# Performance work log

Measured on AMD Instinct MI355X. Metric: run time of the kernel, lower is better.

## Reference

```python
import jax, jax.numpy as jnp
import numpy as np

B, C, D, W, H = 2, 256, 16, 32, 32
CS = 256          # in_channels_style
SN = 256          # number of style tokens
HEADS = 8
DH = C // HEADS
EPS = 1e-6


def setup_inputs() -> dict:
    key = jax.random.key(0)
    ks = jax.random.split(key, 8)
    x = jax.random.normal(ks[0], (B, C, D, W, H), dtype=jnp.float32)
    s = jax.random.normal(ks[1], (B, SN, CS), dtype=jnp.float32)
    # learned parameters
    ln_w = jnp.ones((C,), jnp.float32)
    ln_b = jnp.zeros((C,), jnp.float32)
    lns_w = jnp.ones((CS,), jnp.float32)
    lns_b = jnp.zeros((CS,), jnp.float32)
    sc = 0.02
    Wq = jax.random.normal(ks[2], (C, C), jnp.float32) * sc   # (out, in) 1x1 conv3d
    Wk = jax.random.normal(ks[3], (C, CS), jnp.float32) * sc  # Linear weight (out, in)
    Wv = jax.random.normal(ks[4], (C, CS), jnp.float32) * sc
    Wo = jax.random.normal(ks[5], (C, C), jnp.float32) * sc   # proj_out 1x1 conv3d
    bo = jnp.zeros((C,), jnp.float32)
    return {"x": x, "s": s, "ln_w": ln_w, "ln_b": ln_b, "lns_w": lns_w,
            "lns_b": lns_b, "Wq": Wq, "Wk": Wk, "Wv": Wv, "Wo": Wo, "bo": bo}


def reference(x, s, ln_w, ln_b, lns_w, lns_b, Wq, Wk, Wv, Wo, bo):
    b = x.shape[0]
    # channels_first LayerNorm over channel dim (dim 1) of 5D tensor
    u = x.mean(axis=1, keepdims=True)
    var = ((x - u) ** 2).mean(axis=1, keepdims=True)
    hn = (x - u) / jnp.sqrt(var + EPS)
    hn = ln_w[None, :, None, None, None] * hn + ln_b[None, :, None, None, None]
    # standard LayerNorm on last dim of style tokens
    mu = s.mean(axis=-1, keepdims=True)
    sv = ((s - mu) ** 2).mean(axis=-1, keepdims=True)
    sn = (s - mu) / jnp.sqrt(sv + EPS) * lns_w + lns_b
    # projections: 1x1 conv3d == channel matmul; linears on style
    q = jnp.einsum('bcdwh,oc->bodwh', hn, Wq)               # (B,C,D,W,H)
    k = jnp.einsum('bnc,oc->bon', sn, Wk)                    # (B,C,Sn)
    v = jnp.einsum('bnc,oc->bon', sn, Wv)                    # (B,C,Sn)
    d, w, h = q.shape[2], q.shape[3], q.shape[4]
    N = d * w * h
    q = q.reshape(b * HEADS, DH, N).transpose(0, 2, 1)       # (B*h, N, dh)
    k = k.reshape(b * HEADS, DH, SN)                         # (B*h, dh, Sn)
    v = v.reshape(b * HEADS, DH, SN)                         # (B*h, dh, Sn)
    scores = jnp.einsum('bnd,bds->bns', q, k) * (DH ** -0.5)
    attn = jax.nn.softmax(scores, axis=2)                    # (B*h, N, Sn)
    out = jnp.einsum('bds,bns->bdn', v, attn)                # (B*h, dh, N)
    out = out.reshape(b, C, d, w, h)
    out = jnp.einsum('bcdwh,oc->bodwh', out, Wo) + bo[None, :, None, None, None]
    return x + out
```

## Files before the change

kernel.cpp:

```cpp
#include <hip/hip_runtime.h>

#define EPS_ 1e-6f

typedef __attribute__((ext_vector_type(8))) short bf16x8;
typedef __attribute__((ext_vector_type(4))) float f32x4;

__device__ __forceinline__ unsigned short f2b(float f){
  union { float f; unsigned int u; } v; v.f = f;
  unsigned int r = v.u + 0x7fffu + ((v.u >> 16) & 1u);
  return (unsigned short)(r >> 16);
}
__device__ __forceinline__ unsigned int packrne(float a, float b){
  return (unsigned int)f2b(a) | ((unsigned int)f2b(b) << 16);
}
__device__ __forceinline__ unsigned int packtr(float a, float b){
  return (__float_as_uint(a) >> 16) | (__float_as_uint(b) & 0xffff0000u);
}
union cvt8 { unsigned int u[4]; bf16x8 v; };

__global__ __launch_bounds__(256) void k_prep(
    const float* __restrict__ Wq, const float* __restrict__ Wk,
    const float* __restrict__ Wv, const float* __restrict__ Wo,
    const float* __restrict__ s, const float* __restrict__ lns_w,
    const float* __restrict__ lns_b,
    unsigned short* __restrict__ bWq, unsigned short* __restrict__ bWo,
    unsigned short* __restrict__ Kb, unsigned short* __restrict__ Vb){
  __shared__ unsigned short snb[64*264];
  int t = threadIdx.x;
  int blk = blockIdx.x;
  if (blk < 256){
    int i = blk*256 + t;
    bWq[i] = f2b(Wq[i]);
    bWo[i] = f2b(Wo[i]);
    return;
  }
  int idx = blk - 256;
  int b = idx >> 3, n0 = ((idx >> 1) & 3) * 64, mat = idx & 1;
  int tok = t >> 2, sub = t & 3;
  {
    const float4* srow = (const float4*)(s + ((size_t)(b*256 + n0 + tok))*256 + sub*64);
    float4 vv[16];
    float s1 = 0.f, s2 = 0.f;
    #pragma unroll
    for (int j=0;j<16;++j){
      float4 v = srow[j]; vv[j] = v;
      s1 += (v.x+v.y)+(v.z+v.w);
      s2 += (v.x*v.x+v.y*v.y)+(v.z*v.z+v.w*v.w);
    }
    s1 += __shfl_xor(s1,1); s1 += __shfl_xor(s1,2);
    s2 += __shfl_xor(s2,1); s2 += __shfl_xor(s2,2);
    float mu = s1*(1.f/256.f);
    float rstd = rsqrtf(s2*(1.f/256.f) - mu*mu + EPS_);
    const float4* wr = (const float4*)(lns_w + sub*64);
    const float4* br = (const float4*)(lns_b + sub*64);
    #pragma unroll
    for (int j=0;j<16;++j){
      float4 v = vv[j], g = wr[j], o = br[j];
      float n0v = (v.x-mu)*rstd*g.x + o.x;
      float n1v = (v.y-mu)*rstd*g.y + o.y;
      float n2v = (v.z-mu)*rstd*g.z + o.z;
      float n3v = (v.w-mu)*rstd*g.w + o.w;
      uint2 pk = { packrne(n0v,n1v), packrne(n2v,n3v) };
      *(uint2*)&snb[tok*264 + sub*64 + j*4] = pk;
    }
  }
  __syncthreads();
  int lane = t & 63, w = t >> 6, quad = lane >> 4, l16 = lane & 15;
  const float* W = mat ? Wv : Wk;
  f32x4 acc[4][4];
  #pragma unroll
  for (int ot=0;ot<4;++ot)
    #pragma unroll
    for (int nt=0;nt<4;++nt) acc[ot][nt] = (f32x4){0.f,0.f,0.f,0.f};
  for (int ks=0; ks<8; ++ks){
    bf16x8 afr[4], bfr[4];
    #pragma unroll
    for (int ot=0;ot<4;++ot){
      const float4* wr = (const float4*)(W + (size_t)(w*64 + ot*16 + l16)*256 + ks*32 + quad*8);
      float4 a0 = wr[0], a1 = wr[1];
      cvt8 cv;
      cv.u[0]=packrne(a0.x,a0.y); cv.u[1]=packrne(a0.z,a0.w);
      cv.u[2]=packrne(a1.x,a1.y); cv.u[3]=packrne(a1.z,a1.w);
      afr[ot] = cv.v;
    }
    #pragma unroll
    for (int nt=0;nt<4;++nt)
      bfr[nt] = *(const bf16x8*)&snb[(nt*16+l16)*264 + ks*32 + quad*8];
    #pragma unroll
    for (int ot=0;ot<4;++ot)
      #pragma unroll
      for (int nt=0;nt<4;++nt)
        acc[ot][nt] = __builtin_amdgcn_mfma_f32_16x16x32_bf16(afr[ot], bfr[nt], acc[ot][nt], 0,0,0);
  }
  #pragma unroll
  for (int ot=0;ot<4;++ot){
    int otg = w*4 + ot;
    int h = otg >> 1, dbase = (otg&1)*16 + quad*4;
    #pragma unroll
    for (int nt=0;nt<4;++nt){
      int n = n0 + nt*16 + l16;
      if (!mat){
        uint2 pk = { packrne(acc[ot][nt][0], acc[ot][nt][1]),
                     packrne(acc[ot][nt][2], acc[ot][nt][3]) };
        *(uint2*)&Kb[(((size_t)(b*8+h))*256 + n)*32 + dbase] = pk;
      } else {
        #pragma unroll
        for (int r=0;r<4;++r)
          Vb[(((size_t)(b*8+h))*32 + dbase + r)*256 + n] = f2b(acc[ot][nt][r]);
      }
    }
  }
}

__global__ __launch_bounds__(256,4) void k_mega(
    const float* __restrict__ x, const float* __restrict__ ln_w,
    const float* __restrict__ ln_b,
    const unsigned short* __restrict__ bWq, const unsigned short* __restrict__ bWo,
    const unsigned short* __restrict__ Kb, const unsigned short* __restrict__ Vb,
    const float* __restrict__ bo, float* __restrict__ out){
  __shared__ unsigned short buf1[32*264];
  __shared__ float st[512];
  int t = threadIdx.x;
  int blk = blockIdx.x;
  int b = blk >> 9, p0 = (blk & 511) << 5;
  int pp = t & 31, seg = t >> 5;
  const float* xb = x + ((size_t)b << 22) + p0 + pp;

  float s1=0.f, s2=0.f;
  for (int k=0;k<16;++k){
    int c = seg*32 + 2*k;
    float v0 = xb[(size_t)c << 14], v1 = xb[(size_t)(c+1) << 14];
    s1 += v0+v1; s2 += v0*v0+v1*v1;
    *(unsigned int*)&buf1[pp*264 + c] = packrne(v0, v1);
  }
  st[seg*32+pp] = s1; st[256+seg*32+pp] = s2;
  __syncthreads();
  float a=0.f, q=0.f;
  #pragma unroll
  for (int g=0; g<8; ++g){ a += st[g*32+pp]; q += st[256+g*32+pp]; }
  float mu = a*(1.f/256.f);
  float rstd = rsqrtf(q*(1.f/256.f) - mu*mu + EPS_);
  for (int k=0;k<16;++k){
    int c = seg*32 + 2*k;
    unsigned int pk = *(unsigned int*)&buf1[pp*264 + c];
    float v0 = __uint_as_float(pk << 16);
    float v1 = __uint_as_float(pk & 0xffff0000u);
    v0 = (v0-mu)*rstd*ln_w[c]   + ln_b[c];
    v1 = (v1-mu)*rstd*ln_w[c+1] + ln_b[c+1];
    *(unsigned int*)&buf1[pp*264 + c] = packrne(v0, v1);
  }
  __syncthreads();

  int lane = t & 63, w = t >> 6, quad = lane >> 4, l16 = lane & 15;
  int ptile = w & 1, ohalf = w >> 1;
  int prow = ptile*16 + l16;
  const float qs = 0.17677669529663689f * 1.44269504088896341f;

  {
    f32x4 acc[4][2];
    #pragma unroll
    for (int ot=0;ot<4;++ot)
      #pragma unroll
      for (int pt=0;pt<2;++pt) acc[ot][pt] = (f32x4){0.f,0.f,0.f,0.f};
    const unsigned short* wq = bWq + (size_t)(w*64 + l16)*256 + quad*8;
    #pragma unroll 2
    for (int ks=0; ks<8; ++ks){
      bf16x8 bfr[2], afr[4];
      #pragma unroll
      for (int ot=0;ot<4;++ot)
        afr[ot] = *(const bf16x8*)(wq + (size_t)ot*16*256 + ks*32);
      #pragma unroll
      for (int pt=0;pt<2;++pt)
        bfr[pt] = *(const bf16x8*)&buf1[(pt*16+l16)*264 + ks*32 + quad*8];
      #pragma unroll
      for (int ot=0;ot<4;++ot)
        #pragma unroll
        for (int pt=0;pt<2;++pt)
          acc[ot][pt] = __builtin_amdgcn_mfma_f32_16x16x32_bf16(afr[ot], bfr[pt], acc[ot][pt], 0,0,0);
    }
    __syncthreads();
    #pragma unroll
    for (int ot=0;ot<4;++ot){
      int o = w*64 + ot*16 + quad*4;
      #pragma unroll
      for (int pt=0;pt<2;++pt){
        uint2 pk = { packrne(acc[ot][pt][0]*qs, acc[ot][pt][1]*qs),
                     packrne(acc[ot][pt][2]*qs, acc[ot][pt][3]*qs) };
        *(uint2*)&buf1[(pt*16+l16)*264 + o] = pk;
      }
    }
  }
  __syncthreads();

  int srcA = ((( 2*quad   )&3)<<4) + l16;
  int srcB = (((2*quad + 1)&3)<<4) + l16;
  bool hiq = quad >= 2;
  bf16x8 qf[4];
  #pragma unroll
  for (int hh=0;hh<4;++hh)
    qf[hh] = *(const bf16x8*)&buf1[prow*264 + (ohalf*4+hh)*32 + quad*8];

  for (int hh=0; hh<4; ++hh){
    int h = ohalf*4 + hh;
    int bh = b*8 + h;
    const unsigned short* kb = Kb + (size_t)bh*8192 + quad*8;
    const unsigned short* vb = Vb + (size_t)bh*8192 + quad*8;
    f32x4 av[2] = {{0.f,0.f,0.f,0.f},{0.f,0.f,0.f,0.f}};
    float sm0=0.f, sm1=0.f, sm2=0.f, sm3=0.f;
    #pragma unroll 2
    for (int ks=0; ks<8; ++ks){
      bf16x8 kf0 = *(const bf16x8*)(kb + (size_t)((2*ks  )*16+l16)*32);
      bf16x8 kf1 = *(const bf16x8*)(kb + (size_t)((2*ks+1)*16+l16)*32);
      bf16x8 vf0 = *(const bf16x8*)(vb + (size_t)(     l16)*256 + ks*32);
      bf16x8 vf1 = *(const bf16x8*)(vb + (size_t)(16 + l16)*256 + ks*32);
      f32x4 z = {0.f,0.f,0.f,0.f};
      f32x4 s0 = __builtin_amdgcn_mfma_f32_16x16x32_bf16(kf0, qf[hh], z, 0,0,0);
      f32x4 s1 = __builtin_amdgcn_mfma_f32_16x16x32_bf16(kf1, qf[hh], z, 0,0,0);
      float e00 = exp2f(s0[0]), e01 = exp2f(s0[1]);
      float e02 = exp2f(s0[2]), e03 = exp2f(s0[3]);
      float e10 = exp2f(s1[0]), e11 = exp2f(s1[1]);
      float e12 = exp2f(s1[2]), e13 = exp2f(s1[3]);
      sm0 += e00 + e10; sm1 += e01 + e11;
      sm2 += e02 + e12; sm3 += e03 + e13;
      unsigned int p00 = packtr(e00, e01), p01 = packtr(e02, e03);
      unsigned int p10 = packtr(e10, e11), p11 = packtr(e12, e13);
      unsigned int aA0 = (unsigned int)__shfl((int)p00, srcA);
      unsigned int aB0 = (unsigned int)__shfl((int)p10, srcA);
      unsigned int aA1 = (unsigned int)__shfl((int)p01, srcA);
      unsigned int aB1 = (unsigned int)__shfl((int)p11, srcA);
      unsigned int bA0 = (unsigned int)__shfl((int)p00, srcB);
      unsigned int bB0 = (unsigned int)__shfl((int)p10, srcB);
      unsigned int bA1 = (unsigned int)__shfl((int)p01, srcB);
      unsigned int bB1 = (unsigned int)__shfl((int)p11, srcB);
      cvt8 cv;
      cv.u[0] = hiq ? aB0 : aA0;
      cv.u[1] = hiq ? aB1 : aA1;
      cv.u[2] = hiq ? bB0 : bA0;
      cv.u[3] = hiq ? bB1 : bA1;
      bf16x8 pf = cv.v;
      av[0] = __builtin_amdgcn_mfma_f32_16x16x32_bf16(vf0, pf, av[0], 0,0,0);
      av[1] = __builtin_amdgcn_mfma_f32_16x16x32_bf16(vf1, pf, av[1], 0,0,0);
    }
    float sm = (sm0+sm1)+(sm2+sm3);
    sm += __shfl_xor(sm, 16);
    sm += __shfl_xor(sm, 32);
    float inv = 1.f/sm;
    #pragma unroll
    for (int dt=0; dt<2; ++dt){
      uint2 pko = { packrne(av[dt][0]*inv, av[dt][1]*inv),
                    packrne(av[dt][2]*inv, av[dt][3]*inv) };
      *(uint2*)&buf1[prow*264 + h*32 + dt*16 + quad*4] = pko;
    }
  }
  __syncthreads();

  {
    f32x4 oacc[4][2];
    #pragma unroll
    for (int ot=0;ot<4;++ot)
      #pragma unroll
      for (int pt=0;pt<2;++pt) oacc[ot][pt] = (f32x4){0.f,0.f,0.f,0.f};
    const unsigned short* wo = bWo + (size_t)(w*64 + l16)*256 + quad*8;
    #pragma unroll 2
    for (int ks=0; ks<8; ++ks){
      bf16x8 bfr[2], afr[4];
      #pragma unroll
      for (int ot=0;ot<4;++ot)
        afr[ot] = *(const bf16x8*)(wo + (size_t)ot*16*256 + ks*32);
      #pragma unroll
      for (int pt=0;pt<2;++pt)
        bfr[pt] = *(const bf16x8*)&buf1[(pt*16+l16)*264 + ks*32 + quad*8];
      #pragma unroll
      for (int ot=0;ot<4;++ot)
        #pragma unroll
        for (int pt=0;pt<2;++pt)
          oacc[ot][pt] = __builtin_amdgcn_mfma_f32_16x16x32_bf16(afr[ot], bfr[pt], oacc[ot][pt], 0,0,0);
    }
    #pragma unroll
    for (int ot=0;ot<4;++ot){
      int o = w*64 + ot*16 + quad*4;
      #pragma unroll
      for (int pt=0;pt<2;++pt){
        int p = p0 + pt*16 + l16;
        #pragma unroll
        for (int r=0;r<4;++r){
          size_t idx = (((size_t)b*256 + o + r) << 14) + p;
          out[idx] = oacc[ot][pt][r] + bo[o+r] + x[idx];
        }
      }
    }
  }
}

extern "C" void kernel_launch(void* const* d_in, const int* in_sizes, int n_in,
                              void* d_out, int out_size, void* d_ws, size_t ws_size,
                              hipStream_t stream) {
  const float* x     = (const float*)d_in[0];
  const float* s     = (const float*)d_in[1];
  const float* ln_w  = (const float*)d_in[2];
  const float* ln_b  = (const float*)d_in[3];
  const float* lns_w = (const float*)d_in[4];
  const float* lns_b = (const float*)d_in[5];
  const float* Wq    = (const float*)d_in[6];
  const float* Wk    = (const float*)d_in[7];
  const float* Wv    = (const float*)d_in[8];
  const float* Wo    = (const float*)d_in[9];
  const float* bo    = (const float*)d_in[10];
  float* out = (float*)d_out;

  unsigned short* bWq = (unsigned short*)d_ws;
  unsigned short* bWo = bWq + 65536;
  unsigned short* Kb  = bWo + 65536;
  unsigned short* Vb  = Kb + 131072;

  k_prep<<<272,  256, 0, stream>>>(Wq, Wk, Wv, Wo, s, lns_w, lns_b, bWq, bWo, Kb, Vb);
  k_mega<<<1024, 256, 0, stream>>>(x, ln_w, ln_b, bWq, bWo, Kb, Vb, bo, out);
}
```

Measured before the change: 191.1 us.

## Halve pixel tile per block to raise occupancy and drop a barrier

Shrinks each block's pixel tile from 32 to 16 positions, doubles the grid, and raises launch bounds to 8 blocks per CU. Each wave now handles two heads across all 16 rows instead of four heads on half the rows, so one block barrier after the Q projection can be dropped. The aim is more resident waves to hide memory and MFMA latency. In exchange, the Wq/Wo weight fragments are loaded twice as often per pixel, and the MFMA work per loaded fragment is reduced.

```diff
diff --git a/kernel.cpp b/kernel.cpp
--- a/kernel.cpp
+++ b/kernel.cpp
@@ -112,36 +112,36 @@
   }
 }
 
-__global__ __launch_bounds__(256,4) void k_mega(
+__global__ __launch_bounds__(256,8) void k_mega(
     const float* __restrict__ x, const float* __restrict__ ln_w,
     const float* __restrict__ ln_b,
     const unsigned short* __restrict__ bWq, const unsigned short* __restrict__ bWo,
     const unsigned short* __restrict__ Kb, const unsigned short* __restrict__ Vb,
     const float* __restrict__ bo, float* __restrict__ out){
-  __shared__ unsigned short buf1[32*264];
+  __shared__ unsigned short buf1[16*264];
   __shared__ float st[512];
   int t = threadIdx.x;
   int blk = blockIdx.x;
-  int b = blk >> 9, p0 = (blk & 511) << 5;
-  int pp = t & 31, seg = t >> 5;
+  int b = blk >> 10, p0 = (blk & 1023) << 4;
+  int pp = t & 15, seg = t >> 4;
   const float* xb = x + ((size_t)b << 22) + p0 + pp;
 
   float s1=0.f, s2=0.f;
-  for (int k=0;k<16;++k){
-    int c = seg*32 + 2*k;
+  for (int k=0;k<8;++k){
+    int c = seg*16 + 2*k;
     float v0 = xb[(size_t)c << 14], v1 = xb[(size_t)(c+1) << 14];
     s1 += v0+v1; s2 += v0*v0+v1*v1;
     *(unsigned int*)&buf1[pp*264 + c] = packrne(v0, v1);
   }
-  st[seg*32+pp] = s1; st[256+seg*32+pp] = s2;
+  st[seg*16+pp] = s1; st[256+seg*16+pp] = s2;
   __syncthreads();
   float a=0.f, q=0.f;
   #pragma unroll
-  for (int g=0; g<8; ++g){ a += st[g*32+pp]; q += st[256+g*32+pp]; }
+  for (int g=0; g<16; ++g){ a += st[g*16+pp]; q += st[256+g*16+pp]; }
   float mu = a*(1.f/256.f);
   float rstd = rsqrtf(q*(1.f/256.f) - mu*mu + EPS_);
-  for (int k=0;k<16;++k){
-    int c = seg*32 + 2*k;
+  for (int k=0;k<8;++k){
+    int c = seg*16 + 2*k;
     unsigned int pk = *(unsigned int*)&buf1[pp*264 + c];
     float v0 = __uint_as_float(pk << 16);
     float v1 = __uint_as_float(pk & 0xffff0000u);
@@ -152,56 +152,44 @@
   __syncthreads();
 
   int lane = t & 63, w = t >> 6, quad = lane >> 4, l16 = lane & 15;
-  int ptile = w & 1, ohalf = w >> 1;
-  int prow = ptile*16 + l16;
   const float qs = 0.17677669529663689f * 1.44269504088896341f;
 
   {
-    f32x4 acc[4][2];
-    #pragma unroll
-    for (int ot=0;ot<4;++ot)
-      #pragma unroll
-      for (int pt=0;pt<2;++pt) acc[ot][pt] = (f32x4){0.f,0.f,0.f,0.f};
+    f32x4 acc[4];
+    #pragma unroll
+    for (int ot=0;ot<4;++ot) acc[ot] = (f32x4){0.f,0.f,0.f,0.f};
     const unsigned short* wq = bWq + (size_t)(w*64 + l16)*256 + quad*8;
     #pragma unroll 2
     for (int ks=0; ks<8; ++ks){
-      bf16x8 bfr[2], afr[4];
+      bf16x8 afr[4];
       #pragma unroll
       for (int ot=0;ot<4;++ot)
         afr[ot] = *(const bf16x8*)(wq + (size_t)ot*16*256 + ks*32);
-      #pragma unroll
-      for (int pt=0;pt<2;++pt)
-        bfr[pt] = *(const bf16x8*)&buf1[(pt*16+l16)*264 + ks*32 + quad*8];
-      #pragma unroll
-      for (int ot=0;ot<4;++ot)
-        #pragma unroll
-        for (int pt=0;pt<2;++pt)
-          acc[ot][pt] = __builtin_amdgcn_mfma_f32_16x16x32_bf16(afr[ot], bfr[pt], acc[ot][pt], 0,0,0);
+      bf16x8 bfr = *(const bf16x8*)&buf1[l16*264 + ks*32 + quad*8];
+      #pragma unroll
+      for (int ot=0;ot<4;++ot)
+        acc[ot] = __builtin_amdgcn_mfma_f32_16x16x32_bf16(afr[ot], bfr, acc[ot], 0,0,0);
     }
     __syncthreads();
     #pragma unroll
     for (int ot=0;ot<4;++ot){
       int o = w*64 + ot*16 + quad*4;
-      #pragma unroll
-      for (int pt=0;pt<2;++pt){
-        uint2 pk = { packrne(acc[ot][pt][0]*qs, acc[ot][pt][1]*qs),
-                     packrne(acc[ot][pt][2]*qs, acc[ot][pt][3]*qs) };
-        *(uint2*)&buf1[(pt*16+l16)*264 + o] = pk;
-      }
-    }
-  }
-  __syncthreads();
+      uint2 pk = { packrne(acc[ot][0]*qs, acc[ot][1]*qs),
+                   packrne(acc[ot][2]*qs, acc[ot][3]*qs) };
+      *(uint2*)&buf1[l16*264 + o] = pk;
+    }
+  }
 
   int srcA = ((( 2*quad   )&3)<<4) + l16;
   int srcB = (((2*quad + 1)&3)<<4) + l16;
   bool hiq = quad >= 2;
-  bf16x8 qf[4];
-  #pragma unroll
-  for (int hh=0;hh<4;++hh)
-    qf[hh] = *(const bf16x8*)&buf1[prow*264 + (ohalf*4+hh)*32 + quad*8];
-
-  for (int hh=0; hh<4; ++hh){
-    int h = ohalf*4 + hh;
+  bf16x8 qf[2];
+  #pragma unroll
+  for (int hh=0;hh<2;++hh)
+    qf[hh] = *(const bf16x8*)&buf1[l16*264 + (w*2+hh)*32 + quad*8];
+
+  for (int hh=0; hh<2; ++hh){
+    int h = w*2 + hh;
     int bh = b*8 + h;
     const unsigned short* kb = Kb + (size_t)bh*8192 + quad*8;
     const unsigned short* vb = Vb + (size_t)bh*8192 + quad*8;
@@ -249,44 +237,35 @@
     for (int dt=0; dt<2; ++dt){
       uint2 pko = { packrne(av[dt][0]*inv, av[dt][1]*inv),
                     packrne(av[dt][2]*inv, av[dt][3]*inv) };
-      *(uint2*)&buf1[prow*264 + h*32 + dt*16 + quad*4] = pko;
+      *(uint2*)&buf1[l16*264 + h*32 + dt*16 + quad*4] = pko;
     }
   }
   __syncthreads();
 
   {
-    f32x4 oacc[4][2];
-    #pragma unroll
-    for (int ot=0;ot<4;++ot)
-      #pragma unroll
-      for (int pt=0;pt<2;++pt) oacc[ot][pt] = (f32x4){0.f,0.f,0.f,0.f};
+    f32x4 oacc[4];
+    #pragma unroll
+    for (int ot=0;ot<4;++ot) oacc[ot] = (f32x4){0.f,0.f,0.f,0.f};
     const unsigned short* wo = bWo + (size_t)(w*64 + l16)*256 + quad*8;
     #pragma unroll 2
     for (int ks=0; ks<8; ++ks){
-      bf16x8 bfr[2], afr[4];
+      bf16x8 afr[4];
       #pragma unroll
       for (int ot=0;ot<4;++ot)
         afr[ot] = *(const bf16x8*)(wo + (size_t)ot*16*256 + ks*32);
-      #pragma unroll
-      for (int pt=0;pt<2;++pt)
-        bfr[pt] = *(const bf16x8*)&buf1[(pt*16+l16)*264 + ks*32 + quad*8];
-      #pragma unroll
-      for (int ot=0;ot<4;++ot)
-        #pragma unroll
-        for (int pt=0;pt<2;++pt)
-          oacc[ot][pt] = __builtin_amdgcn_mfma_f32_16x16x32_bf16(afr[ot], bfr[pt], oacc[ot][pt], 0,0,0);
+      bf16x8 bfr = *(const bf16x8*)&buf1[l16*264 + ks*32 + quad*8];
+      #pragma unroll
+      for (int ot=0;ot<4;++ot)
+        oacc[ot] = __builtin_amdgcn_mfma_f32_16x16x32_bf16(afr[ot], bfr, oacc[ot], 0,0,0);
     }
     #pragma unroll
     for (int ot=0;ot<4;++ot){
       int o = w*64 + ot*16 + quad*4;
-      #pragma unroll
-      for (int pt=0;pt<2;++pt){
-        int p = p0 + pt*16 + l16;
-        #pragma unroll
-        for (int r=0;r<4;++r){
-          size_t idx = (((size_t)b*256 + o + r) << 14) + p;
-          out[idx] = oacc[ot][pt][r] + bo[o+r] + x[idx];
-        }
+      int p = p0 + l16;
+      #pragma unroll
+      for (int r=0;r<4;++r){
+        size_t idx = (((size_t)b*256 + o + r) << 14) + p;
+        out[idx] = oacc[ot][r] + bo[o+r] + x[idx];
       }
     }
   }
@@ -314,5 +293,5 @@
   unsigned short* Vb  = Kb + 131072;
 
   k_prep<<<272,  256, 0, stream>>>(Wq, Wk, Wv, Wo, s, lns_w, lns_b, bWq, bWo, Kb, Vb);
-  k_mega<<<1024, 256, 0, stream>>>(x, ln_w, ln_b, bWq, bWo, Kb, Vb, bo, out);
-}
+  k_mega<<<2048, 256, 0, stream>>>(x, ln_w, ln_b, bWq, bWo, Kb, Vb, bo, out);
+}
```

New measurement: 225.1 us. +17.8%, slower.
